# Kernel tuning notes

Hardware: AMD Instinct MI355X
Metric: run time of the kernel (lower is better)

Reference implementation:

```python
import jax, jax.numpy as jnp
import numpy as np

B, T, C, H = 2, 2048, 1024, 16
D = C // H  # head dim = 64

def setup_inputs() -> dict:
    key = jax.random.key(0)
    k1, k2, k3 = jax.random.split(key, 3)
    x = jax.random.normal(k1, (B, T, C), dtype=jnp.float32)
    Wqkv = jax.random.normal(k2, (C, 3 * C), dtype=jnp.float32) * (1.0 / np.sqrt(C))
    bqkv = jnp.zeros((3 * C,), dtype=jnp.float32)
    Wo = jax.random.normal(k3, (C, C), dtype=jnp.float32) * (1.0 / np.sqrt(C))
    bo = jnp.zeros((C,), dtype=jnp.float32)
    return {"x": x, "Wqkv": Wqkv, "bqkv": bqkv, "Wo": Wo, "bo": bo}

def reference(x, Wqkv, bqkv, Wo, bo):
    b, t, c = x.shape
    qkv = x @ Wqkv + bqkv                              # [B,T,3C]
    q, k, v = jnp.split(qkv, 3, axis=-1)
    # [B,T,C] -> [B,H,T,D]
    q = q.reshape(b, t, H, D).transpose(0, 2, 1, 3)
    k = k.reshape(b, t, H, D).transpose(0, 2, 1, 3)
    v = v.reshape(b, t, H, D).transpose(0, 2, 1, 3)
    scores = jnp.einsum('bhqd,bhkd->bhqk', q, k) * (1.0 / np.sqrt(D))
    causal = jnp.tril(jnp.ones((t, t), dtype=bool))
    scores = jnp.where(causal, scores, -jnp.inf)
    probs = jax.nn.softmax(scores, axis=-1)           # dropout p=0 -> identity
    out = jnp.einsum('bhqk,bhkd->bhqd', probs, v)
    out = out.transpose(0, 2, 1, 3).reshape(b, t, c)
    return out @ Wo + bo
```

## Files before the change

### kernel.cpp

```cpp
#include <hip/hip_runtime.h>
#include <hip/hip_bf16.h>

typedef __attribute__((ext_vector_type(8))) short bf16x8;
typedef __attribute__((ext_vector_type(4))) short bf16x4;
typedef __attribute__((ext_vector_type(4))) float f32x4;

static __device__ __forceinline__ __hip_bfloat16 f2b(float f) {
    return __float2bfloat16(f);
}
static __device__ __forceinline__ unsigned pack2(float a, float b) {
    unsigned ua = (unsigned)__bfloat16_as_ushort(__float2bfloat16(a));
    unsigned ub = (unsigned)__bfloat16_as_ushort(__float2bfloat16(b));
    return ua | (ub << 16);
}
static __device__ __forceinline__ float exp2fast(float x) {
    return __builtin_amdgcn_exp2f(x);
}

#define QSCALE 0.1803368801111f

__global__ __launch_bounds__(256) void k_prep(
    const float* __restrict__ x, __hip_bfloat16* __restrict__ xb,
    const float* __restrict__ Wqkv, __hip_bfloat16* __restrict__ WqkvT,
    const float* __restrict__ Wo, __hip_bfloat16* __restrict__ WoT)
{
    const int bx = blockIdx.x;
    if (bx < 2048) {
        int i = bx * 256 + threadIdx.x;
        const int stride = 2048 * 256;
        for (; i < 1048576; i += stride) {
            float4 v = reinterpret_cast<const float4*>(x)[i];
            __hip_bfloat16* o = xb + 4 * (size_t)i;
            o[0] = f2b(v.x); o[1] = f2b(v.y); o[2] = f2b(v.z); o[3] = f2b(v.w);
        }
        return;
    }
    __shared__ float tile[32][33];
    const float* in;
    __hip_bfloat16* outp;
    int R, Cn, c0, r0;
    if (bx < 5120) {
        const int b = bx - 2048;
        in = Wqkv; outp = WqkvT; R = 1024; Cn = 3072;
        c0 = (b % 96) * 32; r0 = (b / 96) * 32;
    } else {
        const int b = bx - 5120;
        in = Wo; outp = WoT; R = 1024; Cn = 1024;
        c0 = (b & 31) * 32; r0 = (b >> 5) * 32;
    }
    const int tx = threadIdx.x & 31, ty = threadIdx.x >> 5;
#pragma unroll
    for (int i = 0; i < 32; i += 8)
        tile[ty + i][tx] = in[(size_t)(r0 + ty + i) * Cn + c0 + tx];
    __syncthreads();
#pragma unroll
    for (int i = 0; i < 32; i += 8)
        outp[(size_t)(c0 + ty + i) * R + r0 + tx] = f2b(tile[tx][ty + i]);
}

#define QK_STAGE(buf, kt)                                                       \
    {                                                                           \
        const int k0_ = (kt) << 5;                                              \
        _Pragma("unroll")                                                       \
        for (int i = 0; i < 2; ++i) {                                           \
            const int idx = i * 256 + tid;                                      \
            const int r_ = idx >> 2;                                            \
            const int j_ = idx & 3;                                             \
            const int js_ = j_ ^ ((r_ >> 1) & 3);                               \
            __builtin_amdgcn_global_load_lds(                                   \
                (const __attribute__((address_space(1))) void*)(A + (size_t)(m0 + r_) * K + k0_ + js_ * 8), \
                (__attribute__((address_space(3))) void*)(&As[buf][r_][j_ * 8]), 16, 0, 0); \
        }                                                                       \
        _Pragma("unroll")                                                       \
        for (int i = 0; i < 2; ++i) {                                           \
            const int idx = i * 256 + tid;                                      \
            const int r_ = idx >> 2;                                            \
            const int j_ = idx & 3;                                             \
            const int js_ = j_ ^ ((r_ >> 1) & 3);                               \
            __builtin_amdgcn_global_load_lds(                                   \
                (const __attribute__((address_space(1))) void*)(Bt + (size_t)(n0 + r_) * K + k0_ + js_ * 8), \
                (__attribute__((address_space(3))) void*)(&Bs[buf][r_][j_ * 8]), 16, 0, 0); \
        }                                                                       \
    }

__global__ __launch_bounds__(256, 3) void k_gemm_qkv(
    const __hip_bfloat16* __restrict__ A,
    const __hip_bfloat16* __restrict__ Bt,
    const float* __restrict__ bias,
    int K,
    __hip_bfloat16* __restrict__ Qb,
    __hip_bfloat16* __restrict__ Kb,
    __hip_bfloat16* __restrict__ Vt)
{
    __shared__ __hip_bfloat16 As[3][128][32];
    __shared__ __hip_bfloat16 Bs[3][128][32];

    const int tid = threadIdx.x;
    const int lane = tid & 63;
    const int wid = tid >> 6;
    const int wm = wid >> 1, wn = wid & 1;
    const int m0 = blockIdx.y * 128, n0 = blockIdx.x * 128;
    const int l15 = lane & 15, lg = lane >> 4;
    const int rchunk = (lg ^ ((l15 >> 1) & 3)) * 8;

    f32x4 acc[4][4] = {};
    const int nt = K >> 5;

    QK_STAGE(0, 0);
    QK_STAGE(1, 1);
    asm volatile("s_waitcnt vmcnt(4)" ::: "memory");
    __builtin_amdgcn_sched_barrier(0);
    __builtin_amdgcn_s_barrier();
    __builtin_amdgcn_sched_barrier(0);

    for (int t = 0; t < nt; ++t) {
        const int cur = t % 3;
        if (t + 2 < nt) {
            const int nxt = (t + 2) % 3;
            QK_STAGE(nxt, t + 2);
        }
        bf16x8 a[4], bb[4];
#pragma unroll
        for (int m = 0; m < 4; ++m)
            a[m] = *(const bf16x8*)&As[cur][wm * 64 + m * 16 + l15][rchunk];
#pragma unroll
        for (int n = 0; n < 4; ++n)
            bb[n] = *(const bf16x8*)&Bs[cur][wn * 64 + n * 16 + l15][rchunk];
        __builtin_amdgcn_s_setprio(1);
#pragma unroll
        for (int m = 0; m < 4; ++m)
#pragma unroll
            for (int n = 0; n < 4; ++n)
                acc[m][n] = __builtin_amdgcn_mfma_f32_16x16x32_bf16(a[m], bb[n], acc[m][n], 0, 0, 0);
        __builtin_amdgcn_s_setprio(0);
        __builtin_amdgcn_sched_barrier(0);
        if (t + 2 < nt)
            asm volatile("s_waitcnt vmcnt(4)" ::: "memory");
        else
            asm volatile("s_waitcnt vmcnt(0)" ::: "memory");
        __builtin_amdgcn_sched_barrier(0);
        __builtin_amdgcn_s_barrier();
        __builtin_amdgcn_sched_barrier(0);
    }

#pragma unroll
    for (int m = 0; m < 4; ++m) {
        const int row = m0 + wm * 64 + m * 16 + lg * 4;
#pragma unroll
        for (int n = 0; n < 4; ++n) {
            const int col = n0 + wn * 64 + n * 16 + l15;
            const float bv = bias[col];
#pragma unroll
            for (int r = 0; r < 4; ++r) {
                const float val = acc[m][n][r] + bv;
                const int rr = row + r;
                const int sec = col >> 10, cw = col & 1023;
                const int hh = cw >> 6, d = cw & 63;
                const int bq = rr >> 11, tt = rr & 2047;
                const int bh = bq * 16 + hh;
                if (sec == 0)
                    Qb[((size_t)bh * 2048 + tt) * 64 + d] = f2b(val * QSCALE);
                else if (sec == 1)
                    Kb[((size_t)bh * 2048 + tt) * 64 + d] = f2b(val);
                else
                    Vt[((size_t)bh * 64 + d) * 2048 + tt] = f2b(val);
            }
        }
    }
}

#define OUT_STAGE(buf, kt)                                                      \
    {                                                                           \
        const int k0_ = (kt) << 5;                                              \
        _Pragma("unroll")                                                       \
        for (int i = 0; i < 2; ++i) {                                           \
            const int idx = i * 256 + tid;                                      \
            const int r_ = idx >> 2;                                            \
            const int j_ = idx & 3;                                             \
            const int js_ = j_ ^ ((r_ >> 1) & 3);                               \
            __builtin_amdgcn_global_load_lds(                                   \
                (const __attribute__((address_space(1))) void*)(A + (size_t)(m0 + r_) * K + k0_ + js_ * 8), \
                (__attribute__((address_space(3))) void*)(&As[buf][r_][j_ * 8]), 16, 0, 0); \
        }                                                                       \
        {                                                                       \
            const int r_ = tid >> 2;                                            \
            const int j_ = tid & 3;                                             \
            const int js_ = j_ ^ ((r_ >> 1) & 3);                               \
            __builtin_amdgcn_global_load_lds(                                   \
                (const __attribute__((address_space(1))) void*)(Bt + (size_t)(n0 + r_) * K + k0_ + js_ * 8), \
                (__attribute__((address_space(3))) void*)(&Bs[buf][r_][j_ * 8]), 16, 0, 0); \
        }                                                                       \
    }

__global__ __launch_bounds__(256, 4) void k_gemm_out(
    const __hip_bfloat16* __restrict__ A,
    const __hip_bfloat16* __restrict__ Bt,
    const float* __restrict__ bias,
    int K, int Nn,
    float* __restrict__ outf)
{
    __shared__ __hip_bfloat16 As[3][128][32];
    __shared__ __hip_bfloat16 Bs[3][64][32];

    const int tid = threadIdx.x;
    const int lane = tid & 63;
    const int wid = tid >> 6;
    const int wm = wid >> 1, wn = wid & 1;
    const int m0 = blockIdx.y * 128, n0 = blockIdx.x * 64;
    const int l15 = lane & 15, lg = lane >> 4;
    const int rchunk = (lg ^ ((l15 >> 1) & 3)) * 8;

    f32x4 acc[4][2] = {};
    const int nt = K >> 5;

    OUT_STAGE(0, 0);
    OUT_STAGE(1, 1);
    asm volatile("s_waitcnt vmcnt(3)" ::: "memory");
    __builtin_amdgcn_sched_barrier(0);
    __builtin_amdgcn_s_barrier();
    __builtin_amdgcn_sched_barrier(0);

    for (int t = 0; t < nt; ++t) {
        const int cur = t % 3;
        if (t + 2 < nt) {
            const int nxt = (t + 2) % 3;
            OUT_STAGE(nxt, t + 2);
        }
        bf16x8 a[4], bb[2];
#pragma unroll
        for (int m = 0; m < 4; ++m)
            a[m] = *(const bf16x8*)&As[cur][wm * 64 + m * 16 + l15][rchunk];
#pragma unroll
        for (int n = 0; n < 2; ++n)
            bb[n] = *(const bf16x8*)&Bs[cur][wn * 32 + n * 16 + l15][rchunk];
        __builtin_amdgcn_s_setprio(1);
#pragma unroll
        for (int m = 0; m < 4; ++m)
#pragma unroll
            for (int n = 0; n < 2; ++n)
                acc[m][n] = __builtin_amdgcn_mfma_f32_16x16x32_bf16(a[m], bb[n], acc[m][n], 0, 0, 0);
        __builtin_amdgcn_s_setprio(0);
        __builtin_amdgcn_sched_barrier(0);
        if (t + 2 < nt)
            asm volatile("s_waitcnt vmcnt(3)" ::: "memory");
        else
            asm volatile("s_waitcnt vmcnt(0)" ::: "memory");
        __builtin_amdgcn_sched_barrier(0);
        __builtin_amdgcn_s_barrier();
        __builtin_amdgcn_sched_barrier(0);
    }

#pragma unroll
    for (int m = 0; m < 4; ++m) {
        const int row = m0 + wm * 64 + m * 16 + lg * 4;
#pragma unroll
        for (int n = 0; n < 2; ++n) {
            const int col = n0 + wn * 32 + n * 16 + l15;
            const float bv = bias[col];
#pragma unroll
            for (int r = 0; r < 4; ++r)
                outf[(size_t)(row + r) * Nn + col] = acc[m][n][r] + bv;
        }
    }
}

#define DEFER_THR 4.0f

#define K_LOAD(BK, KS)                                                          \
    {                                                                           \
        _Pragma("unroll")                                                       \
        for (int kf = 0; kf < 4; ++kf) {                                        \
            const __hip_bfloat16* kp =                                          \
                Kbase + (size_t)((KS) + kf * 16 + l15) * 64 + lg * 8;           \
            BK[kf][0] = *(const bf16x8*)(kp);                                   \
            BK[kf][1] = *(const bf16x8*)(kp + 32);                              \
        }                                                                       \
    }

#define FULL_STEP(BK, BKN, KS)                                                  \
    {                                                                           \
        const int ks_ = (KS);                                                   \
        bf16x8 bv[4][2];                                                        \
        _Pragma("unroll")                                                       \
        for (int dc = 0; dc < 4; ++dc) {                                        \
            const __hip_bfloat16* vp =                                          \
                Vbase + (size_t)(dc * 16 + l15) * 2048 + ks_ + lg * 8;          \
            bv[dc][0] = *(const bf16x8*)(vp);                                   \
            bv[dc][1] = *(const bf16x8*)(vp + 32);                              \
        }                                                                       \
        K_LOAD(BKN, ks_ + 64);                                                  \
        f32x4 s0[4] = {}, s1[4] = {};                                           \
        __builtin_amdgcn_s_setprio(1);                                          \
        _Pragma("unroll")                                                       \
        for (int kf = 0; kf < 4; ++kf) {                                        \
            s0[kf] = __builtin_amdgcn_mfma_f32_16x16x32_bf16(BK[kf][0], aq[0][0], s0[kf], 0, 0, 0); \
            s0[kf] = __builtin_amdgcn_mfma_f32_16x16x32_bf16(BK[kf][1], aq[0][1], s0[kf], 0, 0, 0); \
            s1[kf] = __builtin_amdgcn_mfma_f32_16x16x32_bf16(BK[kf][0], aq[1][0], s1[kf], 0, 0, 0); \
            s1[kf] = __builtin_amdgcn_mfma_f32_16x16x32_bf16(BK[kf][1], aq[1][1], s1[kf], 0, 0, 0); \
        }                                                                       \
        __builtin_amdgcn_s_setprio(0);                                          \
        float px0 = fmaxf(fmaxf(fmaxf(s0[0][0], s0[0][1]), fmaxf(s0[0][2], s0[0][3])), \
                          fmaxf(fmaxf(s0[1][0], s0[1][1]), fmaxf(s0[1][2], s0[1][3]))); \
        px0 = fmaxf(px0, fmaxf(fmaxf(fmaxf(s0[2][0], s0[2][1]), fmaxf(s0[2][2], s0[2][3])), \
                               fmaxf(fmaxf(s0[3][0], s0[3][1]), fmaxf(s0[3][2], s0[3][3])))); \
        float px1 = fmaxf(fmaxf(fmaxf(s1[0][0], s1[0][1]), fmaxf(s1[0][2], s1[0][3])), \
                          fmaxf(fmaxf(s1[1][0], s1[1][1]), fmaxf(s1[1][2], s1[1][3]))); \
        px1 = fmaxf(px1, fmaxf(fmaxf(fmaxf(s1[2][0], s1[2][1]), fmaxf(s1[2][2], s1[2][3])), \
                               fmaxf(fmaxf(s1[3][0], s1[3][1]), fmaxf(s1[3][2], s1[3][3])))); \
        px0 = fmaxf(px0, __shfl_xor(px0, 16));                                  \
        px0 = fmaxf(px0, __shfl_xor(px0, 32));                                  \
        px1 = fmaxf(px1, __shfl_xor(px1, 16));                                  \
        px1 = fmaxf(px1, __shfl_xor(px1, 32));                                  \
        if (__any((px0 > m0 + DEFER_THR) || (px1 > m1 + DEFER_THR))) {          \
            const float mn0 = fmaxf(m0, px0), mn1 = fmaxf(m1, px1);             \
            const float al0 = exp2fast(m0 - mn0), al1 = exp2fast(m1 - mn1);     \
            m0 = mn0; m1 = mn1;                                                 \
            l0 *= al0; l1 *= al1;                                               \
            _Pragma("unroll")                                                   \
            for (int dc = 0; dc < 4; ++dc)                                      \
                _Pragma("unroll")                                               \
                for (int r = 0; r < 4; ++r) {                                   \
                    o[0][dc][r] *= al0;                                         \
                    o[1][dc][r] *= al1;                                         \
                }                                                               \
        }                                                                       \
        float rs0 = 0.f, rs1 = 0.f;                                             \
        _Pragma("unroll")                                                       \
        for (int kf = 0; kf < 4; ++kf) {                                        \
            _Pragma("unroll")                                                   \
            for (int r = 0; r < 4; ++r) {                                       \
                s0[kf][r] = exp2fast(s0[kf][r] - m0);                           \
                s1[kf][r] = exp2fast(s1[kf][r] - m1);                           \
                rs0 += s0[kf][r];                                               \
                rs1 += s1[kf][r];                                               \
            }                                                                   \
            uint2 w0, w1;                                                       \
            w0.x = pack2(s0[kf][0], s0[kf][1]); w0.y = pack2(s0[kf][2], s0[kf][3]); \
            w1.x = pack2(s1[kf][0], s1[kf][1]); w1.y = pack2(s1[kf][2], s1[kf][3]); \
            const int off = l15 * 64 + ((kf * 16 + lg * 4) ^ swz);              \
            *(uint2*)&Pw0[off] = w0;                                            \
            *(uint2*)&Pw1[off] = w1;                                            \
        }                                                                       \
        rs0 += __shfl_xor(rs0, 16); rs0 += __shfl_xor(rs0, 32);                 \
        rs1 += __shfl_xor(rs1, 16); rs1 += __shfl_xor(rs1, 32);                 \
        l0 += rs0; l1 += rs1;                                                   \
        _Pragma("unroll")                                                       \
        for (int c2 = 0; c2 < 2; ++c2) {                                        \
            const int off = l15 * 64 + ((c2 * 32 + lg * 8) ^ swz);              \
            const bf16x8 pb0 = *(const bf16x8*)&Pw0[off];                       \
            const bf16x8 pb1 = *(const bf16x8*)&Pw1[off];                       \
            __builtin_amdgcn_s_setprio(1);                                      \
            _Pragma("unroll")                                                   \
            for (int dc = 0; dc < 4; ++dc) {                                    \
                o[0][dc] = __builtin_amdgcn_mfma_f32_16x16x32_bf16(bv[dc][c2], pb0, o[0][dc], 0, 0, 0); \
                o[1][dc] = __builtin_amdgcn_mfma_f32_16x16x32_bf16(bv[dc][c2], pb1, o[1][dc], 0, 0, 0); \
            }                                                                   \
            __builtin_amdgcn_s_setprio(0);                                      \
        }                                                                       \
    }

#define TAIL_STEP(BK)                                                           \
    {                                                                           \
        const int ks_ = nfull * 64;                                             \
        bf16x8 bv[4][2];                                                        \
        _Pragma("unroll")                                                       \
        for (int dc = 0; dc < 4; ++dc) {                                        \
            const __hip_bfloat16* vp =                                          \
                Vbase + (size_t)(dc * 16 + l15) * 2048 + ks_ + lg * 8;          \
            bv[dc][0] = *(const bf16x8*)(vp);                                   \
            bv[dc][1] = *(const bf16x8*)(vp + 32);                              \
        }                                                                       \
        float mr[2] = {m0, m1}, lr[2] = {l0, l1};                               \
        _Pragma("unroll")                                                       \
        for (int qf = 0; qf < 2; ++qf) {                                        \
            const int qlo = qw + qf * 16;                                       \
            const int qv = qlo + l15;                                           \
            f32x4 s[4] = {};                                                    \
            _Pragma("unroll")                                                   \
            for (int kf = 0; kf < 4; ++kf) {                                    \
                if (ks_ + kf * 16 <= qlo + 15) {                                \
                    s[kf] = __builtin_amdgcn_mfma_f32_16x16x32_bf16(BK[kf][0], aq[qf][0], s[kf], 0, 0, 0); \
                    s[kf] = __builtin_amdgcn_mfma_f32_16x16x32_bf16(BK[kf][1], aq[qf][1], s[kf], 0, 0, 0); \
                }                                                               \
            }                                                                   \
            float p[4][4];                                                      \
            const int kb = ks_ + lg * 4;                                        \
            _Pragma("unroll")                                                   \
            for (int kf = 0; kf < 4; ++kf)                                      \
                _Pragma("unroll")                                               \
                for (int r = 0; r < 4; ++r)                                     \
                    p[kf][r] = (kb + kf * 16 + r <= qv) ? s[kf][r] : -1e30f;    \
            float mx = fmaxf(fmaxf(fmaxf(p[0][0], p[0][1]), fmaxf(p[0][2], p[0][3])), \
                             fmaxf(fmaxf(p[1][0], p[1][1]), fmaxf(p[1][2], p[1][3]))); \
            mx = fmaxf(mx, fmaxf(fmaxf(fmaxf(p[2][0], p[2][1]), fmaxf(p[2][2], p[2][3])), \
                                 fmaxf(fmaxf(p[3][0], p[3][1]), fmaxf(p[3][2], p[3][3])))); \
            mx = fmaxf(mx, __shfl_xor(mx, 16));                                 \
            mx = fmaxf(mx, __shfl_xor(mx, 32));                                 \
            const float mnew = fmaxf(mr[qf], mx);                               \
            const float al = exp2fast(mr[qf] - mnew);                           \
            mr[qf] = mnew;                                                      \
            float rs = 0.f;                                                     \
            _Pragma("unroll")                                                   \
            for (int kf = 0; kf < 4; ++kf)                                      \
                _Pragma("unroll")                                               \
                for (int r = 0; r < 4; ++r) {                                   \
                    p[kf][r] = exp2fast(p[kf][r] - mnew);                       \
                    rs += p[kf][r];                                             \
                }                                                               \
            rs += __shfl_xor(rs, 16);                                           \
            rs += __shfl_xor(rs, 32);                                           \
            lr[qf] = lr[qf] * al + rs;                                          \
            _Pragma("unroll")                                                   \
            for (int dc = 0; dc < 4; ++dc)                                      \
                _Pragma("unroll")                                               \
                for (int r = 0; r < 4; ++r) o[qf][dc][r] *= al;                 \
            __hip_bfloat16* Pw = (qf == 0) ? Pw0 : Pw1;                         \
            _Pragma("unroll")                                                   \
            for (int kf = 0; kf < 4; ++kf) {                                    \
                uint2 w;                                                        \
                w.x = pack2(p[kf][0], p[kf][1]);                                \
                w.y = pack2(p[kf][2], p[kf][3]);                                \
                *(uint2*)&Pw[l15 * 64 + ((kf * 16 + lg * 4) ^ swz)] = w;        \
            }                                                                   \
            _Pragma("unroll")                                                   \
            for (int c2 = 0; c2 < 2; ++c2) {                                    \
                if (ks_ + c2 * 32 <= qlo + 15) {                                \
                    const bf16x8 pb = *(const bf16x8*)&Pw[l15 * 64 + ((c2 * 32 + lg * 8) ^ swz)]; \
                    _Pragma("unroll")                                           \
                    for (int dc = 0; dc < 4; ++dc)                              \
                        o[qf][dc] = __builtin_amdgcn_mfma_f32_16x16x32_bf16(bv[dc][c2], pb, o[qf][dc], 0, 0, 0); \
                }                                                               \
            }                                                                   \
        }                                                                       \
        l0 = lr[0]; l1 = lr[1];                                                 \
    }

__global__ __launch_bounds__(256, 2) void k_attn(
    const __hip_bfloat16* __restrict__ Qb,
    const __hip_bfloat16* __restrict__ Kb,
    const __hip_bfloat16* __restrict__ Vt,
    __hip_bfloat16* __restrict__ att)
{
    __shared__ __hip_bfloat16 P_lds[4][2][16 * 64];
    const int tid = threadIdx.x, lane = tid & 63, wid = tid >> 6;
    const int lid = blockIdx.x;
    const int xcd = lid & 7, j = lid >> 3;
    const int jj = j >> 2;
    const int tile = (jj < 8) ? (15 - jj) : (jj - 8);
    const int bh = xcd * 4 + (j & 3);
    const int q0 = tile * 128;
    const int qw = q0 + wid * 32;
    const int l15 = lane & 15, lg = lane >> 4;
    const int swz = (l15 & 7) << 3;

    const __hip_bfloat16* Qbase = Qb + (size_t)bh * 2048 * 64;
    const __hip_bfloat16* Kbase = Kb + (size_t)bh * 2048 * 64;
    const __hip_bfloat16* Vbase = Vt + (size_t)bh * 64 * 2048;

    bf16x8 aq[2][2];
#pragma unroll
    for (int qf = 0; qf < 2; ++qf)
#pragma unroll
        for (int c = 0; c < 2; ++c)
            aq[qf][c] = *(const bf16x8*)(Qbase + (size_t)(qw + qf * 16 + l15) * 64 + c * 32 + lg * 8);

    f32x4 o[2][4] = {};
    float m0 = -1e30f, m1 = -1e30f, l0 = 0.f, l1 = 0.f;

    const int nfull = qw >> 6;
    __hip_bfloat16* Pw0 = &P_lds[wid][0][0];
    __hip_bfloat16* Pw1 = &P_lds[wid][1][0];

    bf16x8 bkA[4][2], bkB[4][2];
    K_LOAD(bkA, 0);

    if (nfull & 1) {
        FULL_STEP(bkA, bkB, 0);
        for (int t = 1; t < nfull; t += 2) {
            FULL_STEP(bkB, bkA, t * 64);
            FULL_STEP(bkA, bkB, (t + 1) * 64);
        }
        TAIL_STEP(bkB);
    } else {
        for (int t = 0; t < nfull; t += 2) {
            FULL_STEP(bkA, bkB, t * 64);
            FULL_STEP(bkB, bkA, (t + 1) * 64);
        }
        TAIL_STEP(bkA);
    }

    const int bq = bh >> 4, hh = bh & 15;
    const float inv0 = 1.0f / l0, inv1 = 1.0f / l1;
#pragma unroll
    for (int qf = 0; qf < 2; ++qf) {
        const float inv = (qf == 0) ? inv0 : inv1;
        const size_t rowb = ((size_t)(bq * 2048 + qw + qf * 16 + l15)) * 1024 + hh * 64;
#pragma unroll
        for (int dc = 0; dc < 4; ++dc) {
            bf16x4 st;
#pragma unroll
            for (int r = 0; r < 4; ++r)
                st[r] = (short)__bfloat16_as_ushort(__float2bfloat16(o[qf][dc][r] * inv));
            *(bf16x4*)(att + rowb + dc * 16 + lg * 4) = st;
        }
    }
}

extern "C" void kernel_launch(void* const* d_in, const int* in_sizes, int n_in,
                              void* d_out, int out_size, void* d_ws, size_t ws_size,
                              hipStream_t stream)
{
    const float* x    = (const float*)d_in[0];
    const float* Wqkv = (const float*)d_in[1];
    const float* bqkv = (const float*)d_in[2];
    const float* Wo   = (const float*)d_in[3];
    const float* bo   = (const float*)d_in[4];
    float* out = (float*)d_out;

    char* ws = (char*)d_ws;
    const size_t MB = 1024 * 1024;
    __hip_bfloat16* xb    = (__hip_bfloat16*)(ws);
    __hip_bfloat16* WqkvT = (__hip_bfloat16*)(ws + 8 * MB);
    __hip_bfloat16* WoT   = (__hip_bfloat16*)(ws + 14 * MB);
    __hip_bfloat16* Qb    = (__hip_bfloat16*)(ws + 16 * MB);
    __hip_bfloat16* Kb    = (__hip_bfloat16*)(ws + 24 * MB);
    __hip_bfloat16* Vt    = (__hip_bfloat16*)(ws + 32 * MB);
    __hip_bfloat16* att   = (__hip_bfloat16*)(ws + 40 * MB);

    k_prep<<<6144, 256, 0, stream>>>(x, xb, Wqkv, WqkvT, Wo, WoT);

    k_gemm_qkv<<<dim3(24, 32), 256, 0, stream>>>(
        xb, WqkvT, bqkv, 1024, Qb, Kb, Vt);

    k_attn<<<512, 256, 0, stream>>>(Qb, Kb, Vt, att);

    k_gemm_out<<<dim3(16, 32), 256, 0, stream>>>(
        att, WoT, bo, 1024, 1024, out);
}
```

Baseline: 137.2 us.

## Stage K/V tiles in shared LDS via double-buffered global_load_lds

Before this change, each wave in the attention kernel loaded its own K and V fragments straight from global memory into registers. Now the whole block cooperatively copies each 64-key K/V tile into swizzled, double-buffered LDS with async global_load_lds, and the four waves read their fragments from LDS. The goal is to cut the four-fold redundant K/V traffic to L2/HBM and overlap the next tile's load with current compute. In exchange, a block-wide barrier runs every iteration, and waves with fewer causal tiles must idle until the block finishes all NT steps.

```diff
diff --git a/kernel.cpp b/kernel.cpp
--- a/kernel.cpp
+++ b/kernel.cpp
@@ -266,37 +266,47 @@
 
 #define DEFER_THR 4.0f
 
-#define K_LOAD(BK, KS)                                                          \
+#define AT_STAGE(buf, tt)                                                       \
     {                                                                           \
+        const int ks_ = (tt) << 6;                                              \
+        _Pragma("unroll")                                                       \
+        for (int i = 0; i < 2; ++i) {                                           \
+            const int idx = i * 256 + tid;                                      \
+            const int r_ = idx >> 3;                                            \
+            const int j_ = idx & 7;                                             \
+            const int js_ = j_ ^ (r_ & 7);                                      \
+            __builtin_amdgcn_global_load_lds(                                   \
+                (const __attribute__((address_space(1))) void*)(Kbase + (size_t)(ks_ + r_) * 64 + js_ * 8), \
+                (__attribute__((address_space(3))) void*)(&Ks[buf][r_][j_ * 8]), 16, 0, 0); \
+        }                                                                       \
+        _Pragma("unroll")                                                       \
+        for (int i = 0; i < 2; ++i) {                                           \
+            const int idx = i * 256 + tid;                                      \
+            const int r_ = idx >> 3;                                            \
+            const int j_ = idx & 7;                                             \
+            const int js_ = j_ ^ (r_ & 7);                                      \
+            __builtin_amdgcn_global_load_lds(                                   \
+                (const __attribute__((address_space(1))) void*)(Vbase + (size_t)r_ * 2048 + ks_ + js_ * 8), \
+                (__attribute__((address_space(3))) void*)(&Vs[buf][r_][j_ * 8]), 16, 0, 0); \
+        }                                                                       \
+    }
+
+#define FULL_STEP_L(BUF)                                                        \
+    {                                                                           \
+        bf16x8 bk0[4], bk1[4];                                                  \
         _Pragma("unroll")                                                       \
         for (int kf = 0; kf < 4; ++kf) {                                        \
-            const __hip_bfloat16* kp =                                          \
-                Kbase + (size_t)((KS) + kf * 16 + l15) * 64 + lg * 8;           \
-            BK[kf][0] = *(const bf16x8*)(kp);                                   \
-            BK[kf][1] = *(const bf16x8*)(kp + 32);                              \
-        }                                                                       \
-    }
-
-#define FULL_STEP(BK, BKN, KS)                                                  \
-    {                                                                           \
-        const int ks_ = (KS);                                                   \
-        bf16x8 bv[4][2];                                                        \
-        _Pragma("unroll")                                                       \
-        for (int dc = 0; dc < 4; ++dc) {                                        \
-            const __hip_bfloat16* vp =                                          \
-                Vbase + (size_t)(dc * 16 + l15) * 2048 + ks_ + lg * 8;          \
-            bv[dc][0] = *(const bf16x8*)(vp);                                   \
-            bv[dc][1] = *(const bf16x8*)(vp + 32);                              \
-        }                                                                       \
-        K_LOAD(BKN, ks_ + 64);                                                  \
+            bk0[kf] = *(const bf16x8*)&Ks[BUF][kf * 16 + l15][(lg ^ kswz) * 8]; \
+            bk1[kf] = *(const bf16x8*)&Ks[BUF][kf * 16 + l15][((4 + lg) ^ kswz) * 8]; \
+        }                                                                       \
         f32x4 s0[4] = {}, s1[4] = {};                                           \
         __builtin_amdgcn_s_setprio(1);                                          \
         _Pragma("unroll")                                                       \
         for (int kf = 0; kf < 4; ++kf) {                                        \
-            s0[kf] = __builtin_amdgcn_mfma_f32_16x16x32_bf16(BK[kf][0], aq[0][0], s0[kf], 0, 0, 0); \
-            s0[kf] = __builtin_amdgcn_mfma_f32_16x16x32_bf16(BK[kf][1], aq[0][1], s0[kf], 0, 0, 0); \
-            s1[kf] = __builtin_amdgcn_mfma_f32_16x16x32_bf16(BK[kf][0], aq[1][0], s1[kf], 0, 0, 0); \
-            s1[kf] = __builtin_amdgcn_mfma_f32_16x16x32_bf16(BK[kf][1], aq[1][1], s1[kf], 0, 0, 0); \
+            s0[kf] = __builtin_amdgcn_mfma_f32_16x16x32_bf16(bk0[kf], aq[0][0], s0[kf], 0, 0, 0); \
+            s0[kf] = __builtin_amdgcn_mfma_f32_16x16x32_bf16(bk1[kf], aq[0][1], s0[kf], 0, 0, 0); \
+            s1[kf] = __builtin_amdgcn_mfma_f32_16x16x32_bf16(bk0[kf], aq[1][0], s1[kf], 0, 0, 0); \
+            s1[kf] = __builtin_amdgcn_mfma_f32_16x16x32_bf16(bk1[kf], aq[1][1], s1[kf], 0, 0, 0); \
         }                                                                       \
         __builtin_amdgcn_s_setprio(0);                                          \
         float px0 = fmaxf(fmaxf(fmaxf(s0[0][0], s0[0][1]), fmaxf(s0[0][2], s0[0][3])), \
@@ -346,54 +356,55 @@
         l0 += rs0; l1 += rs1;                                                   \
         _Pragma("unroll")                                                       \
         for (int c2 = 0; c2 < 2; ++c2) {                                        \
+            bf16x8 bv[4];                                                       \
+            _Pragma("unroll")                                                   \
+            for (int dc = 0; dc < 4; ++dc)                                      \
+                bv[dc] = *(const bf16x8*)&Vs[BUF][dc * 16 + l15][(((c2 << 2) | lg) ^ kswz) * 8]; \
             const int off = l15 * 64 + ((c2 * 32 + lg * 8) ^ swz);              \
             const bf16x8 pb0 = *(const bf16x8*)&Pw0[off];                       \
             const bf16x8 pb1 = *(const bf16x8*)&Pw1[off];                       \
             __builtin_amdgcn_s_setprio(1);                                      \
             _Pragma("unroll")                                                   \
             for (int dc = 0; dc < 4; ++dc) {                                    \
-                o[0][dc] = __builtin_amdgcn_mfma_f32_16x16x32_bf16(bv[dc][c2], pb0, o[0][dc], 0, 0, 0); \
-                o[1][dc] = __builtin_amdgcn_mfma_f32_16x16x32_bf16(bv[dc][c2], pb1, o[1][dc], 0, 0, 0); \
+                o[0][dc] = __builtin_amdgcn_mfma_f32_16x16x32_bf16(bv[dc], pb0, o[0][dc], 0, 0, 0); \
+                o[1][dc] = __builtin_amdgcn_mfma_f32_16x16x32_bf16(bv[dc], pb1, o[1][dc], 0, 0, 0); \
             }                                                                   \
             __builtin_amdgcn_s_setprio(0);                                      \
         }                                                                       \
     }
 
-#define TAIL_STEP(BK)                                                           \
+#define TAIL_STEP_L(BUF)                                                        \
     {                                                                           \
         const int ks_ = nfull * 64;                                             \
-        bf16x8 bv[4][2];                                                        \
-        _Pragma("unroll")                                                       \
-        for (int dc = 0; dc < 4; ++dc) {                                        \
-            const __hip_bfloat16* vp =                                          \
-                Vbase + (size_t)(dc * 16 + l15) * 2048 + ks_ + lg * 8;          \
-            bv[dc][0] = *(const bf16x8*)(vp);                                   \
-            bv[dc][1] = *(const bf16x8*)(vp + 32);                              \
-        }                                                                       \
         float mr[2] = {m0, m1}, lr[2] = {l0, l1};                               \
         _Pragma("unroll")                                                       \
         for (int qf = 0; qf < 2; ++qf) {                                        \
             const int qlo = qw + qf * 16;                                       \
             const int qv = qlo + l15;                                           \
+            bf16x8 bk0[4], bk1[4];                                              \
+            _Pragma("unroll")                                                   \
+            for (int kf = 0; kf < 4; ++kf) {                                    \
+                bk0[kf] = *(const bf16x8*)&Ks[BUF][kf * 16 + l15][(lg ^ kswz) * 8]; \
+                bk1[kf] = *(const bf16x8*)&Ks[BUF][kf * 16 + l15][((4 + lg) ^ kswz) * 8]; \
+            }                                                                   \
             f32x4 s[4] = {};                                                    \
             _Pragma("unroll")                                                   \
             for (int kf = 0; kf < 4; ++kf) {                                    \
                 if (ks_ + kf * 16 <= qlo + 15) {                                \
-                    s[kf] = __builtin_amdgcn_mfma_f32_16x16x32_bf16(BK[kf][0], aq[qf][0], s[kf], 0, 0, 0); \
-                    s[kf] = __builtin_amdgcn_mfma_f32_16x16x32_bf16(BK[kf][1], aq[qf][1], s[kf], 0, 0, 0); \
+                    s[kf] = __builtin_amdgcn_mfma_f32_16x16x32_bf16(bk0[kf], aq[qf][0], s[kf], 0, 0, 0); \
+                    s[kf] = __builtin_amdgcn_mfma_f32_16x16x32_bf16(bk1[kf], aq[qf][1], s[kf], 0, 0, 0); \
                 }                                                               \
             }                                                                   \
-            float p[4][4];                                                      \
             const int kb = ks_ + lg * 4;                                        \
             _Pragma("unroll")                                                   \
             for (int kf = 0; kf < 4; ++kf)                                      \
                 _Pragma("unroll")                                               \
                 for (int r = 0; r < 4; ++r)                                     \
-                    p[kf][r] = (kb + kf * 16 + r <= qv) ? s[kf][r] : -1e30f;    \
-            float mx = fmaxf(fmaxf(fmaxf(p[0][0], p[0][1]), fmaxf(p[0][2], p[0][3])), \
-                             fmaxf(fmaxf(p[1][0], p[1][1]), fmaxf(p[1][2], p[1][3]))); \
-            mx = fmaxf(mx, fmaxf(fmaxf(fmaxf(p[2][0], p[2][1]), fmaxf(p[2][2], p[2][3])), \
-                                 fmaxf(fmaxf(p[3][0], p[3][1]), fmaxf(p[3][2], p[3][3])))); \
+                    s[kf][r] = (kb + kf * 16 + r <= qv) ? s[kf][r] : -1e30f;    \
+            float mx = fmaxf(fmaxf(fmaxf(s[0][0], s[0][1]), fmaxf(s[0][2], s[0][3])), \
+                             fmaxf(fmaxf(s[1][0], s[1][1]), fmaxf(s[1][2], s[1][3]))); \
+            mx = fmaxf(mx, fmaxf(fmaxf(fmaxf(s[2][0], s[2][1]), fmaxf(s[2][2], s[2][3])), \
+                                 fmaxf(fmaxf(s[3][0], s[3][1]), fmaxf(s[3][2], s[3][3])))); \
             mx = fmaxf(mx, __shfl_xor(mx, 16));                                 \
             mx = fmaxf(mx, __shfl_xor(mx, 32));                                 \
             const float mnew = fmaxf(mr[qf], mx);                               \
@@ -404,8 +415,8 @@
             for (int kf = 0; kf < 4; ++kf)                                      \
                 _Pragma("unroll")                                               \
                 for (int r = 0; r < 4; ++r) {                                   \
-                    p[kf][r] = exp2fast(p[kf][r] - mnew);                       \
-                    rs += p[kf][r];                                             \
+                    s[kf][r] = exp2fast(s[kf][r] - mnew);                       \
+                    rs += s[kf][r];                                             \
                 }                                                               \
             rs += __shfl_xor(rs, 16);                                           \
             rs += __shfl_xor(rs, 32);                                           \
@@ -418,17 +429,21 @@
             _Pragma("unroll")                                                   \
             for (int kf = 0; kf < 4; ++kf) {                                    \
                 uint2 w;                                                        \
-                w.x = pack2(p[kf][0], p[kf][1]);                                \
-                w.y = pack2(p[kf][2], p[kf][3]);                                \
+                w.x = pack2(s[kf][0], s[kf][1]);                                \
+                w.y = pack2(s[kf][2], s[kf][3]);                                \
                 *(uint2*)&Pw[l15 * 64 + ((kf * 16 + lg * 4) ^ swz)] = w;        \
             }                                                                   \
             _Pragma("unroll")                                                   \
             for (int c2 = 0; c2 < 2; ++c2) {                                    \
                 if (ks_ + c2 * 32 <= qlo + 15) {                                \
+                    bf16x8 bv[4];                                               \
+                    _Pragma("unroll")                                           \
+                    for (int dc = 0; dc < 4; ++dc)                              \
+                        bv[dc] = *(const bf16x8*)&Vs[BUF][dc * 16 + l15][(((c2 << 2) | lg) ^ kswz) * 8]; \
                     const bf16x8 pb = *(const bf16x8*)&Pw[l15 * 64 + ((c2 * 32 + lg * 8) ^ swz)]; \
                     _Pragma("unroll")                                           \
                     for (int dc = 0; dc < 4; ++dc)                              \
-                        o[qf][dc] = __builtin_amdgcn_mfma_f32_16x16x32_bf16(bv[dc][c2], pb, o[qf][dc], 0, 0, 0); \
+                        o[qf][dc] = __builtin_amdgcn_mfma_f32_16x16x32_bf16(bv[dc], pb, o[qf][dc], 0, 0, 0); \
                 }                                                               \
             }                                                                   \
         }                                                                       \
@@ -441,6 +456,8 @@
     const __hip_bfloat16* __restrict__ Vt,
     __hip_bfloat16* __restrict__ att)
 {
+    __shared__ __hip_bfloat16 Ks[2][64][64];
+    __shared__ __hip_bfloat16 Vs[2][64][64];
     __shared__ __hip_bfloat16 P_lds[4][2][16 * 64];
     const int tid = threadIdx.x, lane = tid & 63, wid = tid >> 6;
     const int lid = blockIdx.x;
@@ -452,6 +469,7 @@
     const int qw = q0 + wid * 32;
     const int l15 = lane & 15, lg = lane >> 4;
     const int swz = (l15 & 7) << 3;
+    const int kswz = l15 & 7;
 
     const __hip_bfloat16* Qbase = Qb + (size_t)bh * 2048 * 64;
     const __hip_bfloat16* Kbase = Kb + (size_t)bh * 2048 * 64;
@@ -468,25 +486,23 @@
     float m0 = -1e30f, m1 = -1e30f, l0 = 0.f, l1 = 0.f;
 
     const int nfull = qw >> 6;
+    const int NT = 2 * tile + 2;
     __hip_bfloat16* Pw0 = &P_lds[wid][0][0];
     __hip_bfloat16* Pw1 = &P_lds[wid][1][0];
 
-    bf16x8 bkA[4][2], bkB[4][2];
-    K_LOAD(bkA, 0);
-
-    if (nfull & 1) {
-        FULL_STEP(bkA, bkB, 0);
-        for (int t = 1; t < nfull; t += 2) {
-            FULL_STEP(bkB, bkA, t * 64);
-            FULL_STEP(bkA, bkB, (t + 1) * 64);
-        }
-        TAIL_STEP(bkB);
-    } else {
-        for (int t = 0; t < nfull; t += 2) {
-            FULL_STEP(bkA, bkB, t * 64);
-            FULL_STEP(bkB, bkA, (t + 1) * 64);
-        }
-        TAIL_STEP(bkA);
+    AT_STAGE(0, 0);
+    __syncthreads();
+
+    int cur = 0;
+    for (int tt = 0; tt < NT; ++tt) {
+        if (tt + 1 < NT) AT_STAGE(cur ^ 1, tt + 1);
+        if (tt < nfull) {
+            FULL_STEP_L(cur);
+        } else if (tt == nfull) {
+            TAIL_STEP_L(cur);
+        }
+        __syncthreads();
+        cur ^= 1;
     }
 
     const int bq = bh >> 4, hh = bh & 15;
```

After: 127.8 us. 6.9% less time.
